# Kernel optimization log

Measured on AMD Instinct MI355X. Metric: run time of the kernel, lower is better.

## Reference

```python
import jax, jax.numpy as jnp
import numpy as np

N_NODES = 50000
N_EDGES = 800000
D_IN = 64
D_HID = 64
D_OUT = 64


def setup_inputs() -> dict:
    key = jax.random.key(0)
    ks = jax.random.split(key, 10)
    x = jax.random.normal(ks[0], (N_NODES, D_IN), dtype=jnp.float32)
    src = jax.random.randint(ks[1], (N_EDGES,), 0, N_NODES, dtype=jnp.int32)
    dst = jax.random.randint(ks[2], (N_EDGES,), 0, N_NODES, dtype=jnp.int32)
    s = 1.0 / np.sqrt(D_IN)
    W0 = jax.random.uniform(ks[3], (D_IN, D_HID), jnp.float32, -s, s)
    b0 = jnp.zeros((D_HID,), jnp.float32)
    W1 = jax.random.uniform(ks[4], (D_HID, D_HID), jnp.float32, -s, s)
    b1 = jnp.zeros((D_HID,), jnp.float32)
    W2 = jax.random.uniform(ks[5], (D_HID, D_OUT), jnp.float32, -s, s)
    b2 = jnp.zeros((D_OUT,), jnp.float32)
    return {"x": x, "src": src, "dst": dst, "W0": W0, "b0": b0,
            "W1": W1, "b1": b1, "W2": W2, "b2": b2}


def reference(x, src, dst, W0, b0, W1, b1, W2, b2):
    N = x.shape[0]
    # in-degree (constant across layers)
    deg = jax.ops.segment_sum(jnp.ones(src.shape[0], x.dtype), dst, num_segments=N)
    inv = (1.0 / (deg + 1.0))[:, None]  # [N,1] gcn normalizer (deg + self)

    def sage_gcn(h, W, b):
        # gather neighbor feats along edges, scatter-add to destinations
        agg = jax.ops.segment_sum(h[src], dst, num_segments=N)  # [N,d]
        h_neigh = (agg + h) * inv
        return h_neigh @ W + b

    h = sage_gcn(x, W0, b0)
    h = jax.nn.relu(h)
    h = sage_gcn(h, W1, b1)
    h = jax.nn.relu(h)
    h = sage_gcn(h, W2, b2)
    return h
```

## Files before the change

### kernel.cpp

```cpp
#include <hip/hip_runtime.h>
#include <hip/hip_fp16.h>

#define D 64
#define CAP 64

struct alignas(8) half4v { __half2 a, b; };
typedef _Float16 h2_t __attribute__((ext_vector_type(2)));

union v16u {
    float4 f4;
    h2_t   h2[4];
};

__global__ __launch_bounds__(256) void init_cursor_kernel(int* __restrict__ cursor, int N) {
    int i = blockIdx.x * 256 + threadIdx.x;
    if (i < N) cursor[i] = i << 6;
}

__global__ __launch_bounds__(256) void fill_bucket_sliced_kernel(
    const int* __restrict__ src, const int* __restrict__ dst,
    int* __restrict__ cursor, int* __restrict__ col,
    int nE, int slice_size)
{
    const int g  = blockIdx.x & 7;
    const int gb = blockIdx.x >> 3;
    const int lo = g * slice_size;
    const int hi = lo + slice_size;
    int e4 = (gb * 256 + (int)threadIdx.x) * 4;
    if (e4 + 3 < nE) {
        int4 d = *(const int4*)(dst + e4);
        bool m0 = (d.x >= lo) & (d.x < hi);
        bool m1 = (d.y >= lo) & (d.y < hi);
        bool m2 = (d.z >= lo) & (d.z < hi);
        bool m3 = (d.w >= lo) & (d.w < hi);
        if (m0 | m1 | m2 | m3) {
            int4 s = *(const int4*)(src + e4);
            if (m0) { int k = atomicAdd(&cursor[d.x], 1); if (k < ((d.x + 1) << 6)) col[k] = s.x; }
            if (m1) { int k = atomicAdd(&cursor[d.y], 1); if (k < ((d.y + 1) << 6)) col[k] = s.y; }
            if (m2) { int k = atomicAdd(&cursor[d.z], 1); if (k < ((d.z + 1) << 6)) col[k] = s.z; }
            if (m3) { int k = atomicAdd(&cursor[d.w], 1); if (k < ((d.w + 1) << 6)) col[k] = s.w; }
        }
    } else if (e4 < nE) {
        for (int e = e4; e < nE; ++e) {
            int dd = dst[e];
            if (dd >= lo && dd < hi) {
                int k = atomicAdd(&cursor[dd], 1);
                if (k < ((dd + 1) << 6)) col[k] = src[e];
            }
        }
    }
}

template<bool IN32>
__global__ __launch_bounds__(256) void gemm_kernel(
    const void* __restrict__ hin, const float* __restrict__ W,
    __half* __restrict__ g, int N)
{
    const int j   = threadIdx.x & 63;
    const int wid = (blockIdx.x * blockDim.x + threadIdx.x) >> 6;
    const int nw  = (gridDim.x * blockDim.x) >> 6;

    h2_t wp[32];
    #pragma unroll
    for (int kk = 0; kk < 32; ++kk) {
        h2_t p;
        p[0] = (_Float16)W[(2 * kk + 0) * D + j];
        p[1] = (_Float16)W[(2 * kk + 1) * D + j];
        wp[kk] = p;
    }

    if constexpr (IN32) {
        const float4* __restrict__ x4 = (const float4*)hin;
        for (int r = wid; r < N; r += nw) {
            float4 buf[16];
            #pragma unroll
            for (int t = 0; t < 16; ++t) buf[t] = x4[(size_t)r * 16 + t];
            float o0 = 0.0f, o1 = 0.0f;
            #pragma unroll
            for (int t = 0; t < 16; ++t) {
                h2_t p0, p1;
                p0[0] = (_Float16)buf[t].x; p0[1] = (_Float16)buf[t].y;
                p1[0] = (_Float16)buf[t].z; p1[1] = (_Float16)buf[t].w;
                o0 = __builtin_amdgcn_fdot2(p0, wp[2 * t + 0], o0, false);
                o1 = __builtin_amdgcn_fdot2(p1, wp[2 * t + 1], o1, false);
            }
            g[(size_t)r * D + j] = __float2half(o0 + o1);
        }
    } else {
        const float4* __restrict__ hin4 = (const float4*)hin;
        for (int r = wid; r < N; r += nw) {
            v16u buf[8];
            #pragma unroll
            for (int t = 0; t < 8; ++t) buf[t].f4 = hin4[(size_t)r * 8 + t];
            float o0 = 0.0f, o1 = 0.0f;
            #pragma unroll
            for (int t = 0; t < 8; ++t) {
                o0 = __builtin_amdgcn_fdot2(buf[t].h2[0], wp[t * 4 + 0], o0, false);
                o1 = __builtin_amdgcn_fdot2(buf[t].h2[1], wp[t * 4 + 1], o1, false);
                o0 = __builtin_amdgcn_fdot2(buf[t].h2[2], wp[t * 4 + 2], o0, false);
                o1 = __builtin_amdgcn_fdot2(buf[t].h2[3], wp[t * 4 + 3], o1, false);
            }
            g[(size_t)r * D + j] = __float2half(o0 + o1);
        }
    }
}

template<bool OUT_H>
__global__ __launch_bounds__(256, 4) void agg_kernel(
    const __half* __restrict__ g, const int* __restrict__ cursor,
    const int* __restrict__ col, const float* __restrict__ bias,
    void* __restrict__ hout, int N, int do_relu)
{
    const int lane = threadIdx.x & 63;
    const int sub  = lane >> 4;
    const int fq   = lane & 15;
    const int w    = threadIdx.x >> 6;
    const float4 b4 = ((const float4*)bias)[fq];

    const half4v* __restrict__ gh = (const half4v*)g;

    const int nwaves  = gridDim.x * 4;
    const int ngroups = (N + 3) >> 2;
    for (int grp = blockIdx.x * 4 + w; grp < ngroups; grp += nwaves) {
        const int node   = grp * 4 + sub;
        const bool nvalid = node < N;
        const int ncl = nvalid ? node : (N - 1);
        const int rs  = ncl << 6;
        int ce = cursor[ncl];
        ce = (ce < rs + CAP) ? ce : (rs + CAP);
        const int re  = nvalid ? ce : rs;
        const int deg = re - rs;

        float4 a0 = {0,0,0,0}, a1 = {0,0,0,0}, a2 = {0,0,0,0}, a3 = {0,0,0,0};

        for (int e0 = rs; ; e0 += 16) {
            if (__ballot(e0 < re) == 0ULL) break;
            int ee = e0 + fq;
            int idxv = 0;
            if (ee < re) idxv = col[ee];

            half4v rr[16];
            #pragma unroll
            for (int r = 0; r < 16; ++r) {
                int s = __shfl(idxv, (sub << 4) + r);
                rr[r] = gh[(size_t)s * 16 + fq];
            }
            #pragma unroll
            for (int r = 0; r < 16; ++r) {
                float m = (e0 + r < re) ? 1.0f : 0.0f;
                float2 f0 = __half22float2(rr[r].a);
                float2 f1 = __half22float2(rr[r].b);
                float4& a = (r & 3) == 0 ? a0 : (r & 3) == 1 ? a1
                          : (r & 3) == 2 ? a2 : a3;
                a.x = fmaf(m, f0.x, a.x);
                a.y = fmaf(m, f0.y, a.y);
                a.z = fmaf(m, f1.x, a.z);
                a.w = fmaf(m, f1.y, a.w);
            }
        }

        float4 tt;
        tt.x = (a0.x + a1.x) + (a2.x + a3.x);
        tt.y = (a0.y + a1.y) + (a2.y + a3.y);
        tt.z = (a0.z + a1.z) + (a2.z + a3.z);
        tt.w = (a0.w + a1.w) + (a2.w + a3.w);

        half4v sv = gh[(size_t)ncl * 16 + fq];
        float2 s0f = __half22float2(sv.a);
        float2 s1f = __half22float2(sv.b);
        float invd = 1.0f / (float)(deg + 1);
        float ox = fmaf(tt.x + s0f.x, invd, b4.x);
        float oy = fmaf(tt.y + s0f.y, invd, b4.y);
        float oz = fmaf(tt.z + s1f.x, invd, b4.z);
        float ow = fmaf(tt.w + s1f.y, invd, b4.w);
        if (do_relu) {
            ox = fmaxf(ox, 0.0f); oy = fmaxf(oy, 0.0f);
            oz = fmaxf(oz, 0.0f); ow = fmaxf(ow, 0.0f);
        }
        if (nvalid) {
            if constexpr (OUT_H) {
                half4v o;
                o.a = __floats2half2_rn(ox, oy);
                o.b = __floats2half2_rn(oz, ow);
                ((half4v*)hout)[(size_t)node * 16 + fq] = o;
            } else {
                ((float4*)hout)[(size_t)node * 16 + fq] = make_float4(ox, oy, oz, ow);
            }
        }
    }
}

extern "C" void kernel_launch(void* const* d_in, const int* in_sizes, int n_in,
                              void* d_out, int out_size, void* d_ws, size_t ws_size,
                              hipStream_t stream) {
    const float* x   = (const float*)d_in[0];
    const int*   src = (const int*)d_in[1];
    const int*   dst = (const int*)d_in[2];
    const float* W0  = (const float*)d_in[3];
    const float* b0  = (const float*)d_in[4];
    const float* W1  = (const float*)d_in[5];
    const float* b1  = (const float*)d_in[6];
    const float* W2  = (const float*)d_in[7];
    const float* b2  = (const float*)d_in[8];
    float* out = (float*)d_out;

    const int N = in_sizes[0] / D;
    const int E = in_sizes[1];

    char* ws = (char*)d_ws;
    size_t off = 0;
    auto alloc = [&](size_t bytes) -> void* {
        void* p = ws + off;
        off = (off + bytes + 255) & ~(size_t)255;
        return p;
    };
    int*    cursor = (int*)   alloc((size_t)N * sizeof(int));
    int*    col    = (int*)   alloc((size_t)N * CAP * sizeof(int));
    __half* gbuf   = (__half*)alloc((size_t)N * D * sizeof(__half));
    __half* h1     = (__half*)alloc((size_t)N * D * sizeof(__half));
    __half* h2     = (__half*)alloc((size_t)N * D * sizeof(__half));

    const int n_blocks = (N + 255) / 256;
    init_cursor_kernel<<<n_blocks, 256, 0, stream>>>(cursor, N);
    const int e4_blocks = (E / 4 + 255) / 256;
    const int slice_size = (N + 7) / 8;
    fill_bucket_sliced_kernel<<<e4_blocks * 8, 256, 0, stream>>>(src, dst, cursor, col, E, slice_size);

    const int gemm_blocks = 1024;
    const int agg_blocks  = 3136;

    gemm_kernel<true ><<<gemm_blocks, 256, 0, stream>>>(x,  W0, gbuf, N);
    agg_kernel<true ><<<agg_blocks, 256, 0, stream>>>(gbuf, cursor, col, b0, h1,  N, 1);
    gemm_kernel<false><<<gemm_blocks, 256, 0, stream>>>(h1, W1, gbuf, N);
    agg_kernel<true ><<<agg_blocks, 256, 0, stream>>>(gbuf, cursor, col, b1, h2,  N, 1);
    gemm_kernel<false><<<gemm_blocks, 256, 0, stream>>>(h2, W2, gbuf, N);
    agg_kernel<false><<<agg_blocks, 256, 0, stream>>>(gbuf, cursor, col, b2, out, N, 0);
}
```

Measured before the change: 241.2 us.

## Restructure aggregation to one node per wave with 16-byte edge gathers

```diff
diff --git a/kernel.cpp b/kernel.cpp
--- a/kernel.cpp
+++ b/kernel.cpp
@@ -4,8 +4,9 @@
 #define D 64
 #define CAP 64
 
-struct alignas(8) half4v { __half2 a, b; };
 typedef _Float16 h2_t __attribute__((ext_vector_type(2)));
+
+union u4 { float4 f4; __half2 h2[4]; };
 
 union v16u {
     float4 f4;
@@ -112,79 +113,94 @@
     void* __restrict__ hout, int N, int do_relu)
 {
     const int lane = threadIdx.x & 63;
-    const int sub  = lane >> 4;
-    const int fq   = lane & 15;
+    const int og   = lane >> 3;
+    const int fo   = lane & 7;
     const int w    = threadIdx.x >> 6;
-    const float4 b4 = ((const float4*)bias)[fq];
-
-    const half4v* __restrict__ gh = (const half4v*)g;
-
-    const int nwaves  = gridDim.x * 4;
-    const int ngroups = (N + 3) >> 2;
-    for (int grp = blockIdx.x * 4 + w; grp < ngroups; grp += nwaves) {
-        const int node   = grp * 4 + sub;
-        const bool nvalid = node < N;
-        const int ncl = nvalid ? node : (N - 1);
-        const int rs  = ncl << 6;
-        int ce = cursor[ncl];
+
+    const float4 bb0 = ((const float4*)bias)[fo * 2 + 0];
+    const float4 bb1 = ((const float4*)bias)[fo * 2 + 1];
+
+    const float4* __restrict__ g4 = (const float4*)g;
+
+    const int nwaves = gridDim.x * 4;
+    for (int i0 = blockIdx.x * 4 + w; i0 < N; i0 += nwaves) {
+        const int i  = __builtin_amdgcn_readfirstlane(i0);
+        const int rs = i << 6;
+        int ce = cursor[i];
         ce = (ce < rs + CAP) ? ce : (rs + CAP);
-        const int re  = nvalid ? ce : rs;
-        const int deg = re - rs;
-
-        float4 a0 = {0,0,0,0}, a1 = {0,0,0,0}, a2 = {0,0,0,0}, a3 = {0,0,0,0};
-
-        for (int e0 = rs; ; e0 += 16) {
-            if (__ballot(e0 < re) == 0ULL) break;
-            int ee = e0 + fq;
-            int idxv = 0;
-            if (ee < re) idxv = col[ee];
-
-            half4v rr[16];
-            #pragma unroll
-            for (int r = 0; r < 16; ++r) {
-                int s = __shfl(idxv, (sub << 4) + r);
-                rr[r] = gh[(size_t)s * 16 + fq];
-            }
-            #pragma unroll
-            for (int r = 0; r < 16; ++r) {
-                float m = (e0 + r < re) ? 1.0f : 0.0f;
-                float2 f0 = __half22float2(rr[r].a);
-                float2 f1 = __half22float2(rr[r].b);
-                float4& a = (r & 3) == 0 ? a0 : (r & 3) == 1 ? a1
-                          : (r & 3) == 2 ? a2 : a3;
-                a.x = fmaf(m, f0.x, a.x);
-                a.y = fmaf(m, f0.y, a.y);
-                a.z = fmaf(m, f1.x, a.z);
-                a.w = fmaf(m, f1.y, a.w);
-            }
-        }
-
-        float4 tt;
-        tt.x = (a0.x + a1.x) + (a2.x + a3.x);
-        tt.y = (a0.y + a1.y) + (a2.y + a3.y);
-        tt.z = (a0.z + a1.z) + (a2.z + a3.z);
-        tt.w = (a0.w + a1.w) + (a2.w + a3.w);
-
-        half4v sv = gh[(size_t)ncl * 16 + fq];
-        float2 s0f = __half22float2(sv.a);
-        float2 s1f = __half22float2(sv.b);
+        const int deg = ce - rs;
+
+        int ee = rs + lane;
+        int idxv = (ee < ce) ? col[ee] : 0;
+
+        float4 aA0 = {0,0,0,0}, aA1 = {0,0,0,0};
+        float4 aB0 = {0,0,0,0}, aB1 = {0,0,0,0};
+
+        for (int e0 = 0; e0 < deg; e0 += 16) {
+            int sA = __shfl(idxv, e0 + og);
+            int sB = __shfl(idxv, e0 + 8 + og);
+            u4 rA, rB;
+            rA.f4 = g4[(size_t)sA * 8 + fo];
+            rB.f4 = g4[(size_t)sB * 8 + fo];
+            float mA = (e0 + og < deg) ? 1.0f : 0.0f;
+            float mB = (e0 + 8 + og < deg) ? 1.0f : 0.0f;
+            float2 p;
+            p = __half22float2(rA.h2[0]); aA0.x = fmaf(mA, p.x, aA0.x); aA0.y = fmaf(mA, p.y, aA0.y);
+            p = __half22float2(rA.h2[1]); aA0.z = fmaf(mA, p.x, aA0.z); aA0.w = fmaf(mA, p.y, aA0.w);
+            p = __half22float2(rA.h2[2]); aA1.x = fmaf(mA, p.x, aA1.x); aA1.y = fmaf(mA, p.y, aA1.y);
+            p = __half22float2(rA.h2[3]); aA1.z = fmaf(mA, p.x, aA1.z); aA1.w = fmaf(mA, p.y, aA1.w);
+            p = __half22float2(rB.h2[0]); aB0.x = fmaf(mB, p.x, aB0.x); aB0.y = fmaf(mB, p.y, aB0.y);
+            p = __half22float2(rB.h2[1]); aB0.z = fmaf(mB, p.x, aB0.z); aB0.w = fmaf(mB, p.y, aB0.w);
+            p = __half22float2(rB.h2[2]); aB1.x = fmaf(mB, p.x, aB1.x); aB1.y = fmaf(mB, p.y, aB1.y);
+            p = __half22float2(rB.h2[3]); aB1.z = fmaf(mB, p.x, aB1.z); aB1.w = fmaf(mB, p.y, aB1.w);
+        }
+
+        float4 t0, t1;
+        t0.x = aA0.x + aB0.x; t0.y = aA0.y + aB0.y;
+        t0.z = aA0.z + aB0.z; t0.w = aA0.w + aB0.w;
+        t1.x = aA1.x + aB1.x; t1.y = aA1.y + aB1.y;
+        t1.z = aA1.z + aB1.z; t1.w = aA1.w + aB1.w;
+        t0.x += __shfl_xor(t0.x, 8); t0.x += __shfl_xor(t0.x, 16); t0.x += __shfl_xor(t0.x, 32);
+        t0.y += __shfl_xor(t0.y, 8); t0.y += __shfl_xor(t0.y, 16); t0.y += __shfl_xor(t0.y, 32);
+        t0.z += __shfl_xor(t0.z, 8); t0.z += __shfl_xor(t0.z, 16); t0.z += __shfl_xor(t0.z, 32);
+        t0.w += __shfl_xor(t0.w, 8); t0.w += __shfl_xor(t0.w, 16); t0.w += __shfl_xor(t0.w, 32);
+        t1.x += __shfl_xor(t1.x, 8); t1.x += __shfl_xor(t1.x, 16); t1.x += __shfl_xor(t1.x, 32);
+        t1.y += __shfl_xor(t1.y, 8); t1.y += __shfl_xor(t1.y, 16); t1.y += __shfl_xor(t1.y, 32);
+        t1.z += __shfl_xor(t1.z, 8); t1.z += __shfl_xor(t1.z, 16); t1.z += __shfl_xor(t1.z, 32);
+        t1.w += __shfl_xor(t1.w, 8); t1.w += __shfl_xor(t1.w, 16); t1.w += __shfl_xor(t1.w, 32);
+
+        u4 sv; sv.f4 = g4[(size_t)i * 8 + fo];
+        float2 s0 = __half22float2(sv.h2[0]);
+        float2 s1 = __half22float2(sv.h2[1]);
+        float2 s2 = __half22float2(sv.h2[2]);
+        float2 s3 = __half22float2(sv.h2[3]);
         float invd = 1.0f / (float)(deg + 1);
-        float ox = fmaf(tt.x + s0f.x, invd, b4.x);
-        float oy = fmaf(tt.y + s0f.y, invd, b4.y);
-        float oz = fmaf(tt.z + s1f.x, invd, b4.z);
-        float ow = fmaf(tt.w + s1f.y, invd, b4.w);
+        float4 o0, o1;
+        o0.x = fmaf(t0.x + s0.x, invd, bb0.x);
+        o0.y = fmaf(t0.y + s0.y, invd, bb0.y);
+        o0.z = fmaf(t0.z + s1.x, invd, bb0.z);
+        o0.w = fmaf(t0.w + s1.y, invd, bb0.w);
+        o1.x = fmaf(t1.x + s2.x, invd, bb1.x);
+        o1.y = fmaf(t1.y + s2.y, invd, bb1.y);
+        o1.z = fmaf(t1.z + s3.x, invd, bb1.z);
+        o1.w = fmaf(t1.w + s3.y, invd, bb1.w);
         if (do_relu) {
-            ox = fmaxf(ox, 0.0f); oy = fmaxf(oy, 0.0f);
-            oz = fmaxf(oz, 0.0f); ow = fmaxf(ow, 0.0f);
-        }
-        if (nvalid) {
+            o0.x = fmaxf(o0.x, 0.0f); o0.y = fmaxf(o0.y, 0.0f);
+            o0.z = fmaxf(o0.z, 0.0f); o0.w = fmaxf(o0.w, 0.0f);
+            o1.x = fmaxf(o1.x, 0.0f); o1.y = fmaxf(o1.y, 0.0f);
+            o1.z = fmaxf(o1.z, 0.0f); o1.w = fmaxf(o1.w, 0.0f);
+        }
+        if (og == 0) {
             if constexpr (OUT_H) {
-                half4v o;
-                o.a = __floats2half2_rn(ox, oy);
-                o.b = __floats2half2_rn(oz, ow);
-                ((half4v*)hout)[(size_t)node * 16 + fq] = o;
+                u4 o;
+                o.h2[0] = __floats2half2_rn(o0.x, o0.y);
+                o.h2[1] = __floats2half2_rn(o0.z, o0.w);
+                o.h2[2] = __floats2half2_rn(o1.x, o1.y);
+                o.h2[3] = __floats2half2_rn(o1.z, o1.w);
+                ((float4*)hout)[(size_t)i * 8 + fo] = o.f4;
             } else {
-                ((float4*)hout)[(size_t)node * 16 + fq] = make_float4(ox, oy, oz, ow);
+                ((float4*)hout)[(size_t)i * 16 + fo * 2 + 0] = o0;
+                ((float4*)hout)[(size_t)i * 16 + fo * 2 + 1] = o1;
             }
         }
     }
@@ -227,7 +243,7 @@
     fill_bucket_sliced_kernel<<<e4_blocks * 8, 256, 0, stream>>>(src, dst, cursor, col, E, slice_size);
 
     const int gemm_blocks = 1024;
-    const int agg_blocks  = 3136;
+    const int agg_blocks  = 4096;
 
     gemm_kernel<true ><<<gemm_blocks, 256, 0, stream>>>(x,  W0, gbuf, N);
     agg_kernel<true ><<<agg_blocks, 256, 0, stream>>>(gbuf, cursor, col, b0, h1,  N, 1);
```

Result: slower. 248.6 us (+3.1%).
